# Kernel optimization log

Hardware: AMD Instinct MI355X
Metric: run time of the kernel (lower is better)

## Reference

```python
import jax, jax.numpy as jnp
import numpy as np

LAMBDA_1 = 0.1
LAMBDA_2 = 0.1
MAX_ITER = 200
EPS = 1e-5
L = 128   # out_size + 1
D = 512   # in_feature
M = 2048  # in_size


def make_delta(l):
    # second-difference matrix: lower-tri toeplitz of [1,-2,1], with [0,0]=0, [1,0]=-1
    Dm = (jnp.eye(l, dtype=jnp.float32)
          - 2.0 * jnp.eye(l, k=-1, dtype=jnp.float32)
          + jnp.eye(l, k=-2, dtype=jnp.float32))
    return Dm.at[0, 0].set(0.0).at[1, 0].set(-1.0)


def soft_threshold(z, t):
    return jnp.sign(z) * jnp.maximum(jnp.abs(z) - t, 0.0)


def hankel_to_scalar(Mx):
    # average anti-diagonals of an (l, m) matrix -> vector of length l+m-1
    l, m = Mx.shape
    n = l + m - 1
    idx = (jnp.arange(l)[:, None] + jnp.arange(m)[None, :]).reshape(-1)
    sums = jax.ops.segment_sum(Mx.reshape(-1), idx, num_segments=n)
    k = jnp.arange(n)
    counts = jnp.minimum(jnp.minimum(k + 1, n - k), min(l, m)).astype(Mx.dtype)
    return sums / counts


def nrmse(a, b):
    # normalized (relative) L2 error ||a-b|| / ||a||
    return jnp.linalg.norm(a - b) / jnp.linalg.norm(a)


def setup_inputs() -> dict:
    key = jax.random.key(0)
    k1, k2, k3, k4 = jax.random.split(key, 4)
    x = jax.random.normal(k1, (D, M), dtype=jnp.float32)
    part_y = jax.random.normal(k2, (L, M), dtype=jnp.float32)
    mask = (jax.random.uniform(k3, (L, M)) < 0.8).astype(jnp.float32)
    y0 = jax.random.uniform(k4, (L + M - 1,), dtype=jnp.float32)
    return {"x": x, "part_y": part_y, "mask": mask, "y0": y0}


def reference(x, part_y, mask, y0):
    d, m = x.shape
    l = part_y.shape[0]
    Delta = make_delta(l)
    DtD = Delta.T @ Delta
    max_sx = jnp.linalg.svd(x, compute_uv=False)[0] ** 2          # maxeig(x)
    eig = jnp.linalg.svd(Delta, compute_uv=False)[0] ** 2          # maxeig(Delta)
    tau = 1.0 / (2.0 * (max_sx + LAMBDA_1 * eig))
    lam2 = jnp.where(tau * LAMBDA_2 > 0.1, 0.1 / tau, LAMBDA_2)
    thr = tau * lam2
    tail = l - 1

    def update(A, B, a):
        G = LAMBDA_1 * (DtD @ A) + (mask * (A @ x - part_y)) @ x.T
        A_new = soft_threshold(B - tau * G, thr)
        a_new = (1.0 + jnp.sqrt(1.0 + 4.0 * a * a)) / 2.0
        B_new = A + (a - 1.0) / a_new * (A_new - A)
        return A_new, B_new, a_new

    def cond(state):
        _, _, _, _, it, done = state
        return jnp.logical_and(it < MAX_ITER, jnp.logical_not(done))

    def body(state):
        A, B, a, y_k, it, done = state
        A_new, B_new, a_new = update(A, B, a)
        ax = hankel_to_scalar(A_new @ x)
        conv = nrmse(y_k[-tail:], ax[-tail:])
        return (A_new, B_new, a_new, ax, it + 1, conv <= EPS)

    A0 = jnp.zeros((l, d), dtype=x.dtype)
    state0 = (A0, A0, jnp.float32(1.0), y0, jnp.int32(0), jnp.array(False))
    A, _, _, _, _, _ = jax.lax.while_loop(cond, body, state0)
    return (A @ x, A)
```

## Files before the change

kernel.cpp:

```cpp
#include <hip/hip_runtime.h>
#include <math.h>


#define L 128
#define D 512
#define M 2048
#define TAIL (L - 1)
#define MAXIT 200
#define EPSV 1e-5f
#define LAM1 0.1f
#define LAM2C 0.1f
#define LD (L * D)

#define OFF_A     0
#define OFF_BM    131072
#define OFF_R     262144
#define OFF_AX    524288
#define OFF_P     786432
#define OFF_PAR   OFF_P
#define OFF_Q     1048576
#define OFF_DTD   1310720
#define OFF_DP    1327104
#define OFF_DQ    1343488
#define OFF_CTAB  1359872
#define OFF_YPREV 1360128
#define OFF_PART  1360256
#define OFF_WV    1362304
#define OFF_VV    1362816
#define OFF_T64   1363328
#define OFF_Y64   1367424
#define OFF_SCAL  1368448
#define OFF_WD    1368512
#define OFF_WD2   1368640

#define SC_MX    0
#define SC_MXD   24
#define SC_EIGD  44
#define SC_TAU   45
#define SC_THR   46
#define SI_DONE  48
#define SI_PAR   49

__device__ __forceinline__ float delta_elem(int i, int j) {
  if (i == 0) return 0.f;
  if (i == 1) return (j == 0) ? -1.f : (j == 1 ? 1.f : 0.f);
  return (j == i) ? 1.f : (j == i - 1 ? -2.f : (j == i - 2 ? 1.f : 0.f));
}

__global__ __launch_bounds__(256) void k_init(float* __restrict__ ws,
                                              const float* __restrict__ part_y,
                                              const float* __restrict__ mask,
                                              const float* __restrict__ y0) {
  int gid = blockIdx.x * blockDim.x + threadIdx.x;
  int stride = gridDim.x * blockDim.x;
  for (int i = gid; i < 4 * LD; i += stride) ws[OFF_A + i] = 0.f;
  for (int i = gid; i < L * M; i += stride) ws[OFF_R + i] = -mask[i] * part_y[i];
  for (int i = gid; i < L * L; i += stride) {
    int r = i / L, c = i % L;
    float s = 0.f;
    for (int k = 0; k < L; ++k) s += delta_elem(k, r) * delta_elem(k, c);
    ws[OFF_DTD + i] = s;
  }
  if (gid < TAIL) ws[OFF_YPREV + gid] = y0[M + gid];
  if (gid == 0) {
    for (int i = 0; i < 64; ++i) ws[OFF_SCAL + i] = 0.f;
    ws[OFF_SCAL + SC_MXD] = 6.0f;
    float a = 1.f;
    for (int t = 0; t < MAXIT; ++t) {
      float an = (1.f + sqrtf(1.f + 4.f * a * a)) * 0.5f;
      ws[OFF_CTAB + t] = (a - 1.f) / an;
      a = an;
    }
  }
}

__global__ __launch_bounds__(256) void k_xxt(const float* __restrict__ x,
                                             float* __restrict__ ws) {
  int bt = blockIdx.x;
  int r0 = (bt / 16) * 32, c0 = (bt % 16) * 32;
  int rr = threadIdx.x / 32, cl = threadIdx.x % 32;
  int c = c0 + cl;
  const float4* xc = (const float4*)(x + (size_t)c * M);
  float acc[4] = {0.f, 0.f, 0.f, 0.f};
  for (int m4 = 0; m4 < M / 4; ++m4) {
    float4 b = xc[m4];
#pragma unroll
    for (int k = 0; k < 4; ++k) {
      float4 a = ((const float4*)(x + (size_t)(r0 + rr + 8 * k) * M))[m4];
      acc[k] += a.x * b.x + a.y * b.y + a.z * b.z + a.w * b.w;
    }
  }
  float* P = ws + OFF_P;
  float mloc = 0.f;
#pragma unroll
  for (int k = 0; k < 4; ++k) {
    P[(size_t)(r0 + rr + 8 * k) * D + c] = acc[k];
    mloc = fmaxf(mloc, fabsf(acc[k]));
  }
  __shared__ float sm[256];
  sm[threadIdx.x] = mloc; __syncthreads();
  for (int s = 128; s > 0; s >>= 1) {
    if ((int)threadIdx.x < s) sm[threadIdx.x] = fmaxf(sm[threadIdx.x], sm[threadIdx.x + s]);
    __syncthreads();
  }
  if (threadIdx.x == 0) atomicMax((int*)(ws + OFF_SCAL + SC_MX), __float_as_int(sm[0]));
}

template <int N, int TILES>
__global__ __launch_bounds__(256) void k_sq(const float* __restrict__ src,
                                            float* __restrict__ dst,
                                            float* __restrict__ ws,
                                            int slotIn, int slotOut) {
  float sc = 1.0f / ws[OFF_SCAL + slotIn];
  int bt = blockIdx.x;
  int r0 = (bt / TILES) * 32, c0 = (bt % TILES) * 32;
  int rr = threadIdx.x / 32, cl = threadIdx.x % 32;
  int c = c0 + cl;
  const float4* bc = (const float4*)(src + (size_t)c * N);
  float acc[4] = {0.f, 0.f, 0.f, 0.f};
  for (int m4 = 0; m4 < N / 4; ++m4) {
    float4 b = bc[m4];
#pragma unroll
    for (int k = 0; k < 4; ++k) {
      float4 a = ((const float4*)(src + (size_t)(r0 + rr + 8 * k) * N))[m4];
      acc[k] += a.x * b.x + a.y * b.y + a.z * b.z + a.w * b.w;
    }
  }
  float mloc = 0.f;
#pragma unroll
  for (int k = 0; k < 4; ++k) {
    float v = acc[k] * sc * sc;
    dst[(size_t)(r0 + rr + 8 * k) * N + c] = v;
    mloc = fmaxf(mloc, fabsf(v));
  }
  __shared__ float sm[256];
  sm[threadIdx.x] = mloc; __syncthreads();
  for (int s = 128; s > 0; s >>= 1) {
    if ((int)threadIdx.x < s) sm[threadIdx.x] = fmaxf(sm[threadIdx.x], sm[threadIdx.x + s]);
    __syncthreads();
  }
  if (threadIdx.x == 0) atomicMax((int*)(ws + OFF_SCAL + slotOut), __float_as_int(sm[0]));
}

template <int N>
__global__ __launch_bounds__(64) void k_mv(const float* __restrict__ P,
                                           const float* __restrict__ vin,
                                           float* __restrict__ vout, int useVec) {
  int i = blockIdx.x * 64 + threadIdx.x;
  const float4* Pr = (const float4*)(P + (size_t)i * N);
  float acc = 0.f;
  if (useVec) {
    const float4* v4 = (const float4*)vin;
    for (int j = 0; j < N / 4; ++j) {
      float4 a = Pr[j]; float4 b = v4[j];
      acc += a.x * b.x + a.y * b.y + a.z * b.z + a.w * b.w;
    }
  } else {
    for (int j = 0; j < N / 4; ++j) { float4 a = Pr[j]; acc += a.x + a.y + a.z + a.w; }
  }
  vout[i] = acc;
}

__global__ __launch_bounds__(128) void k_xtv(const float* __restrict__ x,
                                             const float* __restrict__ v,
                                             double* __restrict__ t) {
  int m = blockIdx.x * blockDim.x + threadIdx.x;
  double acc = 0.0;
  for (int i = 0; i < D; ++i) acc += (double)x[(size_t)i * M + m] * (double)v[i];
  t[m] = acc;
}

__global__ __launch_bounds__(64) void k_xt(const float* __restrict__ x,
                                           const double* __restrict__ t,
                                           double* __restrict__ y) {
  int i = blockIdx.x * blockDim.x + threadIdx.x;
  double acc = 0.0;
  for (int m = 0; m < M; ++m) acc += (double)x[(size_t)i * M + m] * t[m];
  y[i] = acc;
}

__global__ __launch_bounds__(512) void k_tau(float* __restrict__ ws) {
  const double* y = (const double*)(ws + OFF_Y64);
  const float* v = ws + OFF_VV;
  __shared__ double sn[512], sd[512];
  int i = threadIdx.x;
  double vi = (double)v[i];
  sn[i] = vi * y[i];
  sd[i] = vi * vi;
  __syncthreads();
  for (int s = 256; s > 0; s >>= 1) {
    if (i < s) { sn[i] += sn[i + s]; sd[i] += sd[i + s]; }
    __syncthreads();
  }
  if (i == 0) {
    float max_sx = (float)(sn[0] / sd[0]);
    float eigD = ws[OFF_SCAL + SC_EIGD];
    float tau = 1.0f / (2.0f * (max_sx + LAM1 * eigD));
    float lam2 = (tau * LAM2C > 0.1f) ? 0.1f / tau : LAM2C;
    ws[OFF_SCAL + SC_TAU] = tau;
    ws[OFF_SCAL + SC_THR] = tau * lam2;
  }
}

__global__ __launch_bounds__(128) void k_eigd(float* __restrict__ ws) {
  int i = threadIdx.x;
  const float* DtD = ws + OFF_DTD;
  const float* v = ws + OFF_WD2;
  float acc = 0.f;
  for (int j = 0; j < L; ++j) acc += DtD[i * L + j] * v[j];
  __shared__ float sn[128], sd[128];
  sn[i] = acc * v[i]; sd[i] = v[i] * v[i];
  __syncthreads();
  for (int s = 64; s > 0; s >>= 1) {
    if (i < s) { sn[i] += sn[i + s]; sd[i] += sd[i + s]; }
    __syncthreads();
  }
  if (i == 0) ws[OFF_SCAL + SC_EIGD] = sn[0] / sd[0];
}

__global__ __launch_bounds__(256) void k1p(const float* __restrict__ x,
                                           float* __restrict__ ws, int t) {
  int* iscal = (int*)(ws + OFF_SCAL);
  if (iscal[SI_DONE]) return;
  int chunk = blockIdx.x >> 6;
  int tile = blockIdx.x & 63;
  int rt = tile >> 3, ct = tile & 7;
  int tid = threadIdx.x;
  int w = tid >> 6, lane = tid & 63;
  int r0 = rt * 16 + w * 4;
  int c = ct * 64 + lane;

  if (chunk == 7 && tile == 0 && t >= 1) {
    __shared__ float snum[128], sden[128];
    if (tid < TAIL) {
      float s = 0.f;
#pragma unroll
      for (int slot = 0; slot < 16; ++slot) s += ws[OFF_PART + slot * 128 + tid];
      float ax = s / (float)(TAIL - tid);
      float yp = ws[OFF_YPREV + tid];
      float d = yp - ax;
      snum[tid] = d * d;
      sden[tid] = yp * yp;
      ws[OFF_YPREV + tid] = ax;
    }
    __syncthreads();
    if (tid == 0) {
      float num = 0.f, den = 0.f;
      for (int k = 0; k < TAIL; ++k) { num += snum[k]; den += sden[k]; }
      float conv = sqrtf(num) / sqrtf(den);
      if (conv <= EPSV) { iscal[SI_DONE] = 1; iscal[SI_PAR] = t & 1; }
    }
  }

  float acc0 = 0.f, acc1 = 0.f, acc2 = 0.f, acc3 = 0.f;
  {
    const float4* xr = (const float4*)(x + (size_t)c * M) + chunk * 64;
    const float4* R0 = (const float4*)(ws + OFF_R + (size_t)(r0 + 0) * M) + chunk * 64;
    const float4* R1 = (const float4*)(ws + OFF_R + (size_t)(r0 + 1) * M) + chunk * 64;
    const float4* R2 = (const float4*)(ws + OFF_R + (size_t)(r0 + 2) * M) + chunk * 64;
    const float4* R3 = (const float4*)(ws + OFF_R + (size_t)(r0 + 3) * M) + chunk * 64;
#pragma unroll 4
    for (int i = 0; i < 64; ++i) {
      float4 b = xr[i];
      float4 a0 = R0[i], a1 = R1[i], a2 = R2[i], a3 = R3[i];
      acc0 += a0.x * b.x + a0.y * b.y + a0.z * b.z + a0.w * b.w;
      acc1 += a1.x * b.x + a1.y * b.y + a1.z * b.z + a1.w * b.w;
      acc2 += a2.x * b.x + a2.y * b.y + a2.z * b.z + a2.w * b.w;
      acc3 += a3.x * b.x + a3.y * b.y + a3.z * b.z + a3.w * b.w;
    }
  }
  if (chunk == 7) {
    const float4* D0 = (const float4*)(ws + OFF_DTD + (size_t)(r0 + 0) * L);
    const float4* D1 = (const float4*)(ws + OFF_DTD + (size_t)(r0 + 1) * L);
    const float4* D2 = (const float4*)(ws + OFF_DTD + (size_t)(r0 + 2) * L);
    const float4* D3 = (const float4*)(ws + OFF_DTD + (size_t)(r0 + 3) * L);
    const float* Ab = ws + OFF_A + (size_t)(t & 1) * LD;
    float g0 = 0.f, g1 = 0.f, g2 = 0.f, g3 = 0.f;
#pragma unroll 2
    for (int p4 = 0; p4 < 32; ++p4) {
      float4 d0 = D0[p4], d1 = D1[p4], d2 = D2[p4], d3 = D3[p4];
      float ap0 = Ab[(size_t)(p4 * 4 + 0) * D + c];
      float ap1 = Ab[(size_t)(p4 * 4 + 1) * D + c];
      float ap2 = Ab[(size_t)(p4 * 4 + 2) * D + c];
      float ap3 = Ab[(size_t)(p4 * 4 + 3) * D + c];
      g0 += d0.x * ap0 + d0.y * ap1 + d0.z * ap2 + d0.w * ap3;
      g1 += d1.x * ap0 + d1.y * ap1 + d1.z * ap2 + d1.w * ap3;
      g2 += d2.x * ap0 + d2.y * ap1 + d2.z * ap2 + d2.w * ap3;
      g3 += d3.x * ap0 + d3.y * ap1 + d3.z * ap2 + d3.w * ap3;
    }
    acc0 += LAM1 * g0; acc1 += LAM1 * g1; acc2 += LAM1 * g2; acc3 += LAM1 * g3;
  }
  float* P = ws + OFF_PAR + (size_t)chunk * LD;
  P[(size_t)(r0 + 0) * D + c] = acc0;
  P[(size_t)(r0 + 1) * D + c] = acc1;
  P[(size_t)(r0 + 2) * D + c] = acc2;
  P[(size_t)(r0 + 3) * D + c] = acc3;
}

__global__ __launch_bounds__(256) void k1b(float* __restrict__ ws, int t) {
  int* iscal = (int*)(ws + OFF_SCAL);
  if (iscal[SI_DONE]) return;
  int idx = blockIdx.x * 256 + threadIdx.x;
  float g = 0.f;
#pragma unroll
  for (int ch = 0; ch < 8; ++ch) g += ws[OFF_PAR + ch * LD + idx];
  float tau = ws[OFF_SCAL + SC_TAU];
  float thr = ws[OFF_SCAL + SC_THR];
  float ctv = ws[OFF_CTAB + t];
  float aold = ws[OFF_A + (t & 1) * LD + idx];
  float bm = ws[OFF_BM + (t & 1) * LD + idx];
  float z = bm - tau * g;
  float az = fabsf(z) - thr;
  float anew = az > 0.f ? copysignf(az, z) : 0.f;
  ws[OFF_A + ((t + 1) & 1) * LD + idx] = anew;
  ws[OFF_BM + ((t + 1) & 1) * LD + idx] = aold + ctv * (anew - aold);
}

__global__ __launch_bounds__(512) void k2(const float* __restrict__ x,
                                          const float* __restrict__ py,
                                          const float* __restrict__ mask,
                                          float* __restrict__ ws, int t) {
  int* iscal = (int*)(ws + OFF_SCAL);
  if (iscal[SI_DONE]) return;
  int bid = blockIdx.x;
  int rt = bid >> 5, ct = bid & 31;
  int tid = threadIdx.x;
  int half = tid >> 8;
  int w2 = (tid >> 6) & 3;
  int lane = tid & 63;
  int r0 = rt * 16 + w2 * 4;
  int c = ct * 64 + lane;
  const float* A = ws + OFF_A + (size_t)((t + 1) & 1) * LD;
  float acc0 = 0.f, acc1 = 0.f, acc2 = 0.f, acc3 = 0.f;
  int d4lo = half * 64;
#pragma unroll 2
  for (int d4 = d4lo; d4 < d4lo + 64; ++d4) {
    float xs0 = x[(size_t)(d4 * 4 + 0) * M + c];
    float xs1 = x[(size_t)(d4 * 4 + 1) * M + c];
    float xs2 = x[(size_t)(d4 * 4 + 2) * M + c];
    float xs3 = x[(size_t)(d4 * 4 + 3) * M + c];
    float4 a0 = ((const float4*)(A + (size_t)(r0 + 0) * D))[d4];
    float4 a1 = ((const float4*)(A + (size_t)(r0 + 1) * D))[d4];
    float4 a2 = ((const float4*)(A + (size_t)(r0 + 2) * D))[d4];
    float4 a3 = ((const float4*)(A + (size_t)(r0 + 3) * D))[d4];
    acc0 += a0.x * xs0 + a0.y * xs1 + a0.z * xs2 + a0.w * xs3;
    acc1 += a1.x * xs0 + a1.y * xs1 + a1.z * xs2 + a1.w * xs3;
    acc2 += a2.x * xs0 + a2.y * xs1 + a2.z * xs2 + a2.w * xs3;
    acc3 += a3.x * xs0 + a3.y * xs1 + a3.z * xs2 + a3.w * xs3;
  }
  __shared__ float tile[16][65];
  if (half == 0) {
    tile[w2 * 4 + 0][lane] = acc0;
    tile[w2 * 4 + 1][lane] = acc1;
    tile[w2 * 4 + 2][lane] = acc2;
    tile[w2 * 4 + 3][lane] = acc3;
  }
  __syncthreads();
  if (half == 1) {
    float s0 = tile[w2 * 4 + 0][lane] + acc0;
    float s1 = tile[w2 * 4 + 1][lane] + acc1;
    float s2 = tile[w2 * 4 + 2][lane] + acc2;
    float s3 = tile[w2 * 4 + 3][lane] + acc3;
    size_t o0 = (size_t)(r0 + 0) * M + c;
    size_t o1 = (size_t)(r0 + 1) * M + c;
    size_t o2 = (size_t)(r0 + 2) * M + c;
    size_t o3 = (size_t)(r0 + 3) * M + c;
    ws[OFF_AX + o0] = s0; ws[OFF_R + o0] = mask[o0] * (s0 - py[o0]);
    ws[OFF_AX + o1] = s1; ws[OFF_R + o1] = mask[o1] * (s1 - py[o1]);
    ws[OFF_AX + o2] = s2; ws[OFF_R + o2] = mask[o2] * (s2 - py[o2]);
    ws[OFF_AX + o3] = s3; ws[OFF_R + o3] = mask[o3] * (s3 - py[o3]);
    tile[w2 * 4 + 0][lane] = s0;
    tile[w2 * 4 + 1][lane] = s1;
    tile[w2 * 4 + 2][lane] = s2;
    tile[w2 * 4 + 3][lane] = s3;
  }
  if (ct >= 30) {
    __syncthreads();
    int slot = rt * 2 + (ct - 30);
    if (tid < TAIL) {
      int kk = M + tid;
      int rbase = rt * 16, c0 = ct * 64;
      int rlo = max(rbase, kk - (c0 + 63));
      int rhi = min(rbase + 15, kk - c0);
      float s = 0.f;
      for (int r = rlo; r <= rhi; ++r) s += tile[r - rbase][(kk - r) - c0];
      ws[OFF_PART + slot * 128 + tid] = s;
    }
  }
}

__global__ __launch_bounds__(256) void k_final(const float* __restrict__ ws,
                                               float* __restrict__ out) {
  const int* iscal = (const int*)(ws + OFF_SCAL);
  int par = iscal[SI_PAR];
  int gid = blockIdx.x * blockDim.x + threadIdx.x;
  int stride = gridDim.x * blockDim.x;
  for (int i = gid; i < L * M; i += stride) out[i] = ws[OFF_AX + i];
  for (int i = gid; i < LD; i += stride) out[L * M + i] = ws[OFF_A + par * LD + i];
}

extern "C" void kernel_launch(void* const* d_in, const int* in_sizes, int n_in,
                              void* d_out, int out_size, void* d_ws, size_t ws_size,
                              hipStream_t stream) {
  (void)in_sizes; (void)n_in; (void)out_size; (void)ws_size;
  const float* x = (const float*)d_in[0];
  const float* py = (const float*)d_in[1];
  const float* mk = (const float*)d_in[2];
  const float* y0 = (const float*)d_in[3];
  float* out = (float*)d_out;
  float* ws = (float*)d_ws;

  float* gP = ws + OFF_P;
  float* gQ = ws + OFF_Q;
  float* dP = ws + OFF_DP;
  float* dQ = ws + OFF_DQ;
  float* gDtD = ws + OFF_DTD;

  k_init<<<256, 256, 0, stream>>>(ws, py, mk, y0);

  k_xxt<<<256, 256, 0, stream>>>(x, ws);
  for (int s = 0; s < 12; ++s) {
    const float* src = (s % 2 == 0) ? gP : gQ;
    float* dst = (s % 2 == 0) ? gQ : gP;
    k_sq<512, 16><<<256, 256, 0, stream>>>(src, dst, ws, SC_MX + s, SC_MX + s + 1);
  }
  k_mv<512><<<8, 64, 0, stream>>>(gP, nullptr, ws + OFF_WV, 0);
  k_mv<512><<<8, 64, 0, stream>>>(gP, ws + OFF_WV, ws + OFF_VV, 1);
  k_mv<512><<<8, 64, 0, stream>>>(gP, ws + OFF_VV, ws + OFF_WV, 1);
  k_mv<512><<<8, 64, 0, stream>>>(gP, ws + OFF_WV, ws + OFF_VV, 1);
  k_xtv<<<16, 128, 0, stream>>>(x, ws + OFF_VV, (double*)(ws + OFF_T64));
  k_xt<<<8, 64, 0, stream>>>(x, (const double*)(ws + OFF_T64), (double*)(ws + OFF_Y64));

  for (int s = 0; s < 10; ++s) {
    const float* src = (s == 0) ? gDtD : ((s % 2 == 1) ? dP : dQ);
    float* dst = (s % 2 == 0) ? dP : dQ;
    k_sq<128, 4><<<16, 256, 0, stream>>>(src, dst, ws, SC_MXD + s, SC_MXD + s + 1);
  }
  k_mv<128><<<2, 64, 0, stream>>>(dQ, nullptr, ws + OFF_WD, 0);
  k_mv<128><<<2, 64, 0, stream>>>(dQ, ws + OFF_WD, ws + OFF_WD2, 2);
  k_eigd<<<1, 128, 0, stream>>>(ws);
  k_tau<<<1, 512, 0, stream>>>(ws);

  for (int t = 0; t < MAXIT; ++t) {
    k1p<<<512, 256, 0, stream>>>(x, ws, t);
    k1b<<<256, 256, 0, stream>>>(ws, t);
    k2<<<256, 512, 0, stream>>>(x, py, mk, ws, t);
  }

  k_final<<<256, 256, 0, stream>>>(ws, out);
}
```

Baseline: 12.38 ms.

## Fuse setup and iteration loop into persistent kernels with grid barriers

Replaces the long sequence of small launches (setup squarings, power iterations, and three kernels per FISTA iteration) with two persistent kernels, k_setup and k_loop. These use a software grid barrier built on atomics over 256 blocks of 512 threads. The gradient is recomputed per output tile with split-K inside the block instead of partial buffers plus a reduction kernel. The goal is to remove launch overhead and the partial-sum round trips. The risk is that the spin barrier deadlocks if not all 256 blocks are co-resident, and the barriers themselves add latency.

```diff
diff --git a/kernel.cpp b/kernel.cpp
--- a/kernel.cpp
+++ b/kernel.cpp
@@ -11,13 +11,14 @@
 #define LAM1 0.1f
 #define LAM2C 0.1f
 #define LD (L * D)
+#define NBLK 256
+#define NTHR 512
 
 #define OFF_A     0
 #define OFF_BM    131072
 #define OFF_R     262144
 #define OFF_AX    524288
 #define OFF_P     786432
-#define OFF_PAR   OFF_P
 #define OFF_Q     1048576
 #define OFF_DTD   1310720
 #define OFF_DP    1327104
@@ -30,8 +31,6 @@
 #define OFF_T64   1363328
 #define OFF_Y64   1367424
 #define OFF_SCAL  1368448
-#define OFF_WD    1368512
-#define OFF_WD2   1368640
 
 #define SC_MX    0
 #define SC_MXD   24
@@ -39,12 +38,33 @@
 #define SC_TAU   45
 #define SC_THR   46
 #define SI_DONE  48
-#define SI_PAR   49
+#define SI_CNT   52
+#define SI_GEN   53
 
 __device__ __forceinline__ float delta_elem(int i, int j) {
   if (i == 0) return 0.f;
   if (i == 1) return (j == 0) ? -1.f : (j == 1 ? 1.f : 0.f);
   return (j == i) ? 1.f : (j == i - 1 ? -2.f : (j == i - 2 ? 1.f : 0.f));
+}
+
+__device__ __forceinline__ void gbar(float* ws) {
+  __syncthreads();
+  if (threadIdx.x == 0) {
+    unsigned* cnt = (unsigned*)(ws + OFF_SCAL) + SI_CNT;
+    unsigned* gen = (unsigned*)(ws + OFF_SCAL) + SI_GEN;
+    __threadfence();
+    unsigned g = __hip_atomic_load(gen, __ATOMIC_RELAXED, __HIP_MEMORY_SCOPE_AGENT);
+    unsigned a = __hip_atomic_fetch_add(cnt, 1u, __ATOMIC_ACQ_REL, __HIP_MEMORY_SCOPE_AGENT);
+    if (a == NBLK - 1) {
+      __hip_atomic_store(cnt, 0u, __ATOMIC_RELAXED, __HIP_MEMORY_SCOPE_AGENT);
+      __hip_atomic_store(gen, g + 1u, __ATOMIC_RELEASE, __HIP_MEMORY_SCOPE_AGENT);
+    } else {
+      while (__hip_atomic_load(gen, __ATOMIC_ACQUIRE, __HIP_MEMORY_SCOPE_AGENT) == g)
+        __builtin_amdgcn_s_sleep(2);
+    }
+    __threadfence();
+  }
+  __syncthreads();
 }
 
 __global__ __launch_bounds__(256) void k_init(float* __restrict__ ws,
@@ -74,329 +94,347 @@
   }
 }
 
-__global__ __launch_bounds__(256) void k_xxt(const float* __restrict__ x,
-                                             float* __restrict__ ws) {
-  int bt = blockIdx.x;
-  int r0 = (bt / 16) * 32, c0 = (bt % 16) * 32;
-  int rr = threadIdx.x / 32, cl = threadIdx.x % 32;
-  int c = c0 + cl;
-  const float4* xc = (const float4*)(x + (size_t)c * M);
-  float acc[4] = {0.f, 0.f, 0.f, 0.f};
-  for (int m4 = 0; m4 < M / 4; ++m4) {
-    float4 b = xc[m4];
-#pragma unroll
-    for (int k = 0; k < 4; ++k) {
-      float4 a = ((const float4*)(x + (size_t)(r0 + rr + 8 * k) * M))[m4];
-      acc[k] += a.x * b.x + a.y * b.y + a.z * b.z + a.w * b.w;
-    }
-  }
-  float* P = ws + OFF_P;
-  float mloc = 0.f;
-#pragma unroll
-  for (int k = 0; k < 4; ++k) {
-    P[(size_t)(r0 + rr + 8 * k) * D + c] = acc[k];
-    mloc = fmaxf(mloc, fabsf(acc[k]));
-  }
-  __shared__ float sm[256];
-  sm[threadIdx.x] = mloc; __syncthreads();
-  for (int s = 128; s > 0; s >>= 1) {
-    if ((int)threadIdx.x < s) sm[threadIdx.x] = fmaxf(sm[threadIdx.x], sm[threadIdx.x + s]);
-    __syncthreads();
-  }
-  if (threadIdx.x == 0) atomicMax((int*)(ws + OFF_SCAL + SC_MX), __float_as_int(sm[0]));
-}
-
 template <int N, int TILES>
-__global__ __launch_bounds__(256) void k_sq(const float* __restrict__ src,
-                                            float* __restrict__ dst,
-                                            float* __restrict__ ws,
-                                            int slotIn, int slotOut) {
-  float sc = 1.0f / ws[OFF_SCAL + slotIn];
-  int bt = blockIdx.x;
+__device__ __forceinline__ void sq_step(const float* __restrict__ src,
+                                        float* __restrict__ dst,
+                                        float* __restrict__ scal,
+                                        int si, int so, float* sm, int bt) {
+  float sc = 1.0f / scal[si];
   int r0 = (bt / TILES) * 32, c0 = (bt % TILES) * 32;
-  int rr = threadIdx.x / 32, cl = threadIdx.x % 32;
+  int rr = threadIdx.x >> 5, cl = threadIdx.x & 31;
   int c = c0 + cl;
   const float4* bc = (const float4*)(src + (size_t)c * N);
-  float acc[4] = {0.f, 0.f, 0.f, 0.f};
+  const float4* a0p = (const float4*)(src + (size_t)(r0 + rr) * N);
+  const float4* a1p = (const float4*)(src + (size_t)(r0 + rr + 16) * N);
+  float a0 = 0.f, a1 = 0.f;
   for (int m4 = 0; m4 < N / 4; ++m4) {
     float4 b = bc[m4];
-#pragma unroll
-    for (int k = 0; k < 4; ++k) {
-      float4 a = ((const float4*)(src + (size_t)(r0 + rr + 8 * k) * N))[m4];
-      acc[k] += a.x * b.x + a.y * b.y + a.z * b.z + a.w * b.w;
-    }
-  }
-  float mloc = 0.f;
-#pragma unroll
-  for (int k = 0; k < 4; ++k) {
-    float v = acc[k] * sc * sc;
-    dst[(size_t)(r0 + rr + 8 * k) * N + c] = v;
-    mloc = fmaxf(mloc, fabsf(v));
-  }
-  __shared__ float sm[256];
-  sm[threadIdx.x] = mloc; __syncthreads();
-  for (int s = 128; s > 0; s >>= 1) {
-    if ((int)threadIdx.x < s) sm[threadIdx.x] = fmaxf(sm[threadIdx.x], sm[threadIdx.x + s]);
-    __syncthreads();
-  }
-  if (threadIdx.x == 0) atomicMax((int*)(ws + OFF_SCAL + slotOut), __float_as_int(sm[0]));
-}
-
-template <int N>
-__global__ __launch_bounds__(64) void k_mv(const float* __restrict__ P,
-                                           const float* __restrict__ vin,
-                                           float* __restrict__ vout, int useVec) {
-  int i = blockIdx.x * 64 + threadIdx.x;
-  const float4* Pr = (const float4*)(P + (size_t)i * N);
-  float acc = 0.f;
-  if (useVec) {
-    const float4* v4 = (const float4*)vin;
-    for (int j = 0; j < N / 4; ++j) {
-      float4 a = Pr[j]; float4 b = v4[j];
-      acc += a.x * b.x + a.y * b.y + a.z * b.z + a.w * b.w;
-    }
-  } else {
-    for (int j = 0; j < N / 4; ++j) { float4 a = Pr[j]; acc += a.x + a.y + a.z + a.w; }
-  }
-  vout[i] = acc;
-}
-
-__global__ __launch_bounds__(128) void k_xtv(const float* __restrict__ x,
-                                             const float* __restrict__ v,
-                                             double* __restrict__ t) {
-  int m = blockIdx.x * blockDim.x + threadIdx.x;
-  double acc = 0.0;
-  for (int i = 0; i < D; ++i) acc += (double)x[(size_t)i * M + m] * (double)v[i];
-  t[m] = acc;
-}
-
-__global__ __launch_bounds__(64) void k_xt(const float* __restrict__ x,
-                                           const double* __restrict__ t,
-                                           double* __restrict__ y) {
-  int i = blockIdx.x * blockDim.x + threadIdx.x;
-  double acc = 0.0;
-  for (int m = 0; m < M; ++m) acc += (double)x[(size_t)i * M + m] * t[m];
-  y[i] = acc;
-}
-
-__global__ __launch_bounds__(512) void k_tau(float* __restrict__ ws) {
-  const double* y = (const double*)(ws + OFF_Y64);
-  const float* v = ws + OFF_VV;
-  __shared__ double sn[512], sd[512];
-  int i = threadIdx.x;
-  double vi = (double)v[i];
-  sn[i] = vi * y[i];
-  sd[i] = vi * vi;
+    float4 p = a0p[m4], q = a1p[m4];
+    a0 += p.x * b.x + p.y * b.y + p.z * b.z + p.w * b.w;
+    a1 += q.x * b.x + q.y * b.y + q.z * b.z + q.w * b.w;
+  }
+  a0 *= sc * sc; a1 *= sc * sc;
+  dst[(size_t)(r0 + rr) * N + c] = a0;
+  dst[(size_t)(r0 + rr + 16) * N + c] = a1;
+  sm[threadIdx.x] = fmaxf(fabsf(a0), fabsf(a1));
   __syncthreads();
   for (int s = 256; s > 0; s >>= 1) {
-    if (i < s) { sn[i] += sn[i + s]; sd[i] += sd[i + s]; }
-    __syncthreads();
-  }
-  if (i == 0) {
-    float max_sx = (float)(sn[0] / sd[0]);
-    float eigD = ws[OFF_SCAL + SC_EIGD];
-    float tau = 1.0f / (2.0f * (max_sx + LAM1 * eigD));
-    float lam2 = (tau * LAM2C > 0.1f) ? 0.1f / tau : LAM2C;
-    ws[OFF_SCAL + SC_TAU] = tau;
-    ws[OFF_SCAL + SC_THR] = tau * lam2;
-  }
-}
-
-__global__ __launch_bounds__(128) void k_eigd(float* __restrict__ ws) {
-  int i = threadIdx.x;
-  const float* DtD = ws + OFF_DTD;
-  const float* v = ws + OFF_WD2;
-  float acc = 0.f;
-  for (int j = 0; j < L; ++j) acc += DtD[i * L + j] * v[j];
-  __shared__ float sn[128], sd[128];
-  sn[i] = acc * v[i]; sd[i] = v[i] * v[i];
-  __syncthreads();
-  for (int s = 64; s > 0; s >>= 1) {
-    if (i < s) { sn[i] += sn[i + s]; sd[i] += sd[i + s]; }
-    __syncthreads();
-  }
-  if (i == 0) ws[OFF_SCAL + SC_EIGD] = sn[0] / sd[0];
-}
-
-__global__ __launch_bounds__(256) void k1p(const float* __restrict__ x,
-                                           float* __restrict__ ws, int t) {
+    if ((int)threadIdx.x < s) sm[threadIdx.x] = fmaxf(sm[threadIdx.x], sm[threadIdx.x + s]);
+    __syncthreads();
+  }
+  if (threadIdx.x == 0) atomicMax((int*)(scal + so), __float_as_int(sm[0]));
+}
+
+__global__ __launch_bounds__(NTHR, 2) void k_setup(const float* __restrict__ x,
+                                                   float* __restrict__ ws) {
+  const int tid = threadIdx.x, bid = blockIdx.x;
+  __shared__ float sm[NTHR];
+  __shared__ double sdn[NTHR], sdd[NTHR];
+  float* scal = ws + OFF_SCAL;
+
+  {
+    int r0 = (bid >> 4) * 32, c0 = (bid & 15) * 32;
+    int rr = tid >> 5, cl = tid & 31;
+    int c = c0 + cl;
+    const float4* xc = (const float4*)(x + (size_t)c * M);
+    const float4* xr0 = (const float4*)(x + (size_t)(r0 + rr) * M);
+    const float4* xr1 = (const float4*)(x + (size_t)(r0 + rr + 16) * M);
+    float a0 = 0.f, a1 = 0.f;
+    for (int m4 = 0; m4 < M / 4; ++m4) {
+      float4 b = xc[m4];
+      float4 p = xr0[m4], q = xr1[m4];
+      a0 += p.x * b.x + p.y * b.y + p.z * b.z + p.w * b.w;
+      a1 += q.x * b.x + q.y * b.y + q.z * b.z + q.w * b.w;
+    }
+    float* P = ws + OFF_P;
+    P[(size_t)(r0 + rr) * D + c] = a0;
+    P[(size_t)(r0 + rr + 16) * D + c] = a1;
+    sm[tid] = fmaxf(fabsf(a0), fabsf(a1));
+    __syncthreads();
+    for (int s = 256; s > 0; s >>= 1) {
+      if (tid < s) sm[tid] = fmaxf(sm[tid], sm[tid + s]);
+      __syncthreads();
+    }
+    if (tid == 0) atomicMax((int*)(scal + SC_MX), __float_as_int(sm[0]));
+  }
+  gbar(ws);
+
+  for (int s = 0; s < 12; ++s) {
+    if (bid < 16 && s < 10) {
+      const float* src = (s == 0) ? ws + OFF_DTD : ((s & 1) ? ws + OFF_DP : ws + OFF_DQ);
+      float* dst = (s & 1) ? ws + OFF_DQ : ws + OFF_DP;
+      sq_step<128, 4>(src, dst, scal, SC_MXD + s, SC_MXD + s + 1, sm, bid);
+    }
+    __syncthreads();
+    {
+      const float* src = (s & 1) ? ws + OFF_Q : ws + OFF_P;
+      float* dst = (s & 1) ? ws + OFF_P : ws + OFF_Q;
+      sq_step<512, 16>(src, dst, scal, SC_MX + s, SC_MX + s + 1, sm, bid);
+    }
+    gbar(ws);
+  }
+
+  const float* gP = ws + OFF_P;
+  const float* dQ = ws + OFF_DQ;
+  if (bid == 0) {
+    const float4* Pr = (const float4*)(gP + (size_t)tid * D);
+    float a = 0.f;
+    for (int j = 0; j < D / 4; ++j) { float4 v = Pr[j]; a += v.x + v.y + v.z + v.w; }
+    ws[OFF_WV + tid] = a;
+  }
+  if (bid == 1 && tid < L) {
+    const float4* Dr = (const float4*)(dQ + (size_t)tid * L);
+    float a = 0.f;
+    for (int j = 0; j < L / 4; ++j) { float4 v = Dr[j]; a += v.x + v.y + v.z + v.w; }
+    ws[OFF_WV + 512 + tid] = a;
+  }
+  gbar(ws);
+  if (bid == 0) {
+    const float4* Pr = (const float4*)(gP + (size_t)tid * D);
+    const float4* v4 = (const float4*)(ws + OFF_WV);
+    float a = 0.f;
+    for (int j = 0; j < D / 4; ++j) {
+      float4 p = Pr[j]; float4 v = v4[j];
+      a += p.x * v.x + p.y * v.y + p.z * v.z + p.w * v.w;
+    }
+    ws[OFF_VV + tid] = a;
+  }
+  if (bid == 1 && tid < L) {
+    const float* wd = ws + OFF_WV + 512;
+    const float* Dr = dQ + (size_t)tid * L;
+    float a = 0.f;
+    for (int j = 0; j < L; ++j) a += Dr[j] * wd[j];
+    ws[OFF_WV + 640 + tid] = a;
+  }
+  gbar(ws);
+  if (bid == 0) {
+    const float4* Pr = (const float4*)(gP + (size_t)tid * D);
+    const float4* v4 = (const float4*)(ws + OFF_VV);
+    float a = 0.f;
+    for (int j = 0; j < D / 4; ++j) {
+      float4 p = Pr[j]; float4 v = v4[j];
+      a += p.x * v.x + p.y * v.y + p.z * v.z + p.w * v.w;
+    }
+    ws[OFF_WV + tid] = a;
+  }
+  if (bid == 1) {
+    float accv = 0.f, vv = 0.f;
+    if (tid < L) {
+      const float* v = ws + OFF_WV + 640;
+      const float* DtD = ws + OFF_DTD;
+      for (int j = 0; j < L; ++j) accv += DtD[(size_t)tid * L + j] * v[j];
+      vv = v[tid];
+    }
+    sm[tid] = (tid < L) ? accv * vv : 0.f;
+    sm[256 + (tid & 255)] = 0.f;
+    __syncthreads();
+    if (tid < L) sm[256 + tid] = vv * vv;
+    __syncthreads();
+    if (tid == 0) {
+      float n = 0.f, d = 0.f;
+      for (int k = 0; k < L; ++k) { n += sm[k]; d += sm[256 + k]; }
+      scal[SC_EIGD] = n / d;
+    }
+  }
+  gbar(ws);
+  if (bid == 0) {
+    const float4* Pr = (const float4*)(gP + (size_t)tid * D);
+    const float4* v4 = (const float4*)(ws + OFF_WV);
+    float a = 0.f;
+    for (int j = 0; j < D / 4; ++j) {
+      float4 p = Pr[j]; float4 v = v4[j];
+      a += p.x * v.x + p.y * v.y + p.z * v.z + p.w * v.w;
+    }
+    ws[OFF_VV + tid] = a;
+  }
+  gbar(ws);
+  if (bid < 4) {
+    int m = bid * NTHR + tid;
+    double acc = 0.0;
+    for (int i = 0; i < D; ++i) acc += (double)x[(size_t)i * M + m] * (double)ws[OFF_VV + i];
+    ((double*)(ws + OFF_T64))[m] = acc;
+  }
+  gbar(ws);
+  if (bid == 0) {
+    const double* t64 = (const double*)(ws + OFF_T64);
+    double acc = 0.0;
+    for (int m = 0; m < M; ++m) acc += (double)x[(size_t)tid * M + m] * t64[m];
+    ((double*)(ws + OFF_Y64))[tid] = acc;
+  }
+  gbar(ws);
+  if (bid == 0) {
+    const double* y = (const double*)(ws + OFF_Y64);
+    double vi = (double)ws[OFF_VV + tid];
+    sdn[tid] = vi * y[tid];
+    sdd[tid] = vi * vi;
+    __syncthreads();
+    for (int s = 256; s > 0; s >>= 1) {
+      if (tid < s) { sdn[tid] += sdn[tid + s]; sdd[tid] += sdd[tid + s]; }
+      __syncthreads();
+    }
+    if (tid == 0) {
+      float max_sx = (float)(sdn[0] / sdd[0]);
+      float eigD = scal[SC_EIGD];
+      float tau = 1.0f / (2.0f * (max_sx + LAM1 * eigD));
+      float lam2 = (tau * LAM2C > 0.1f) ? 0.1f / tau : LAM2C;
+      scal[SC_TAU] = tau;
+      scal[SC_THR] = tau * lam2;
+    }
+  }
+}
+
+__global__ __launch_bounds__(NTHR, 2) void k_loop(const float* __restrict__ x,
+                                                  const float* __restrict__ py,
+                                                  const float* __restrict__ mask,
+                                                  float* __restrict__ ws,
+                                                  float* __restrict__ out) {
+  __shared__ float g2buf[256];
+  __shared__ float tile[16][65];
+  __shared__ float snum[128], sden[128];
+  __shared__ int flag;
+  const int tid = threadIdx.x, bid = blockIdx.x;
   int* iscal = (int*)(ws + OFF_SCAL);
-  if (iscal[SI_DONE]) return;
-  int chunk = blockIdx.x >> 6;
-  int tile = blockIdx.x & 63;
-  int rt = tile >> 3, ct = tile & 7;
-  int tid = threadIdx.x;
-  int w = tid >> 6, lane = tid & 63;
-  int r0 = rt * 16 + w * 4;
-  int c = ct * 64 + lane;
-
-  if (chunk == 7 && tile == 0 && t >= 1) {
-    __shared__ float snum[128], sden[128];
-    if (tid < TAIL) {
-      float s = 0.f;
+  const float tau = ws[OFF_SCAL + SC_TAU];
+  const float thr = ws[OFF_SCAL + SC_THR];
+  int par = 0;
+
+  for (int t = 0; t < MAXIT; ++t) {
+    if (bid == 0 && t >= 1) {
+      if (tid < TAIL) {
+        float s = 0.f;
 #pragma unroll
-      for (int slot = 0; slot < 16; ++slot) s += ws[OFF_PART + slot * 128 + tid];
-      float ax = s / (float)(TAIL - tid);
-      float yp = ws[OFF_YPREV + tid];
-      float d = yp - ax;
-      snum[tid] = d * d;
-      sden[tid] = yp * yp;
-      ws[OFF_YPREV + tid] = ax;
-    }
-    __syncthreads();
-    if (tid == 0) {
-      float num = 0.f, den = 0.f;
-      for (int k = 0; k < TAIL; ++k) { num += snum[k]; den += sden[k]; }
-      float conv = sqrtf(num) / sqrtf(den);
-      if (conv <= EPSV) { iscal[SI_DONE] = 1; iscal[SI_PAR] = t & 1; }
-    }
-  }
-
-  float acc0 = 0.f, acc1 = 0.f, acc2 = 0.f, acc3 = 0.f;
+        for (int slot = 0; slot < 16; ++slot) s += ws[OFF_PART + slot * 128 + tid];
+        float ax = s / (float)(TAIL - tid);
+        float yp = ws[OFF_YPREV + tid];
+        float d0 = yp - ax;
+        snum[tid] = d0 * d0;
+        sden[tid] = yp * yp;
+        ws[OFF_YPREV + tid] = ax;
+      }
+      __syncthreads();
+      if (tid == 0) {
+        float num = 0.f, den = 0.f;
+        for (int k = 0; k < TAIL; ++k) { num += snum[k]; den += sden[k]; }
+        float conv = sqrtf(num) / sqrtf(den);
+        if (conv <= EPSV) iscal[SI_DONE] = 1;
+      }
+      __syncthreads();
+    }
+    {
+      int rt = bid >> 4, ct = bid & 15;
+      int oi = tid & 255;
+      int r = rt * 8 + (oi >> 5);
+      int c = ct * 32 + (oi & 31);
+      int half = tid >> 8;
+      const float4* Rp = (const float4*)(ws + OFF_R + (size_t)r * M) + half * 256;
+      const float4* Xp = (const float4*)(x + (size_t)c * M) + half * 256;
+      float a0 = 0.f, a1 = 0.f;
+#pragma unroll 4
+      for (int i = 0; i < 256; i += 2) {
+        float4 ra = Rp[i], xa = Xp[i];
+        float4 rb = Rp[i + 1], xb = Xp[i + 1];
+        a0 += ra.x * xa.x + ra.y * xa.y + ra.z * xa.z + ra.w * xa.w;
+        a1 += rb.x * xb.x + rb.y * xb.y + rb.z * xb.z + rb.w * xb.w;
+      }
+      float g2 = a0 + a1;
+      if (half) g2buf[oi] = g2;
+      __syncthreads();
+      if (!half) {
+        const float* Ao = ws + OFF_A + (size_t)(t & 1) * LD;
+        const float4* Dr = (const float4*)(ws + OFF_DTD + (size_t)r * L);
+        float gd = 0.f;
+#pragma unroll 4
+        for (int p4 = 0; p4 < 32; ++p4) {
+          float4 dv = Dr[p4];
+          gd += dv.x * Ao[(size_t)(p4 * 4 + 0) * D + c] + dv.y * Ao[(size_t)(p4 * 4 + 1) * D + c] +
+                dv.z * Ao[(size_t)(p4 * 4 + 2) * D + c] + dv.w * Ao[(size_t)(p4 * 4 + 3) * D + c];
+        }
+        float g = g2 + g2buf[oi] + LAM1 * gd;
+        float ctv = ws[OFF_CTAB + t];
+        size_t off = (size_t)r * D + c;
+        float aold = Ao[off];
+        float bm = ws[OFF_BM + (size_t)(t & 1) * LD + off];
+        float z = bm - tau * g;
+        float az = fabsf(z) - thr;
+        float anew = az > 0.f ? copysignf(az, z) : 0.f;
+        ws[OFF_A + (size_t)((t + 1) & 1) * LD + off] = anew;
+        ws[OFF_BM + (size_t)((t + 1) & 1) * LD + off] = aold + ctv * (anew - aold);
+      }
+    }
+    gbar(ws);
+    if (tid == 0) flag = __hip_atomic_load(iscal + SI_DONE, __ATOMIC_RELAXED, __HIP_MEMORY_SCOPE_AGENT);
+    __syncthreads();
+    if (flag) { par = t & 1; break; }
+    {
+      int rt = bid >> 5, ct = bid & 31;
+      int half = tid >> 8, w2 = (tid >> 6) & 3, lane = tid & 63;
+      int r0 = rt * 16 + w2 * 4;
+      int c = ct * 64 + lane;
+      const float* A = ws + OFF_A + (size_t)((t + 1) & 1) * LD;
+      float acc0 = 0.f, acc1 = 0.f, acc2 = 0.f, acc3 = 0.f;
+      int d4lo = half * 64;
+#pragma unroll 2
+      for (int d4 = d4lo; d4 < d4lo + 64; ++d4) {
+        float xs0 = x[(size_t)(d4 * 4 + 0) * M + c];
+        float xs1 = x[(size_t)(d4 * 4 + 1) * M + c];
+        float xs2 = x[(size_t)(d4 * 4 + 2) * M + c];
+        float xs3 = x[(size_t)(d4 * 4 + 3) * M + c];
+        float4 a0v = ((const float4*)(A + (size_t)(r0 + 0) * D))[d4];
+        float4 a1v = ((const float4*)(A + (size_t)(r0 + 1) * D))[d4];
+        float4 a2v = ((const float4*)(A + (size_t)(r0 + 2) * D))[d4];
+        float4 a3v = ((const float4*)(A + (size_t)(r0 + 3) * D))[d4];
+        acc0 += a0v.x * xs0 + a0v.y * xs1 + a0v.z * xs2 + a0v.w * xs3;
+        acc1 += a1v.x * xs0 + a1v.y * xs1 + a1v.z * xs2 + a1v.w * xs3;
+        acc2 += a2v.x * xs0 + a2v.y * xs1 + a2v.z * xs2 + a2v.w * xs3;
+        acc3 += a3v.x * xs0 + a3v.y * xs1 + a3v.z * xs2 + a3v.w * xs3;
+      }
+      if (half == 0) {
+        tile[w2 * 4 + 0][lane] = acc0;
+        tile[w2 * 4 + 1][lane] = acc1;
+        tile[w2 * 4 + 2][lane] = acc2;
+        tile[w2 * 4 + 3][lane] = acc3;
+      }
+      __syncthreads();
+      if (half == 1) {
+        float s0 = tile[w2 * 4 + 0][lane] + acc0;
+        float s1 = tile[w2 * 4 + 1][lane] + acc1;
+        float s2 = tile[w2 * 4 + 2][lane] + acc2;
+        float s3 = tile[w2 * 4 + 3][lane] + acc3;
+        size_t o0 = (size_t)(r0 + 0) * M + c;
+        size_t o1 = (size_t)(r0 + 1) * M + c;
+        size_t o2 = (size_t)(r0 + 2) * M + c;
+        size_t o3 = (size_t)(r0 + 3) * M + c;
+        ws[OFF_AX + o0] = s0; ws[OFF_R + o0] = mask[o0] * (s0 - py[o0]);
+        ws[OFF_AX + o1] = s1; ws[OFF_R + o1] = mask[o1] * (s1 - py[o1]);
+        ws[OFF_AX + o2] = s2; ws[OFF_R + o2] = mask[o2] * (s2 - py[o2]);
+        ws[OFF_AX + o3] = s3; ws[OFF_R + o3] = mask[o3] * (s3 - py[o3]);
+        tile[w2 * 4 + 0][lane] = s0;
+        tile[w2 * 4 + 1][lane] = s1;
+        tile[w2 * 4 + 2][lane] = s2;
+        tile[w2 * 4 + 3][lane] = s3;
+      }
+      if (ct >= 30) {
+        __syncthreads();
+        int slot = rt * 2 + (ct - 30);
+        if (tid < TAIL) {
+          int kk = M + tid;
+          int rbase = rt * 16, c0 = ct * 64;
+          int rlo = max(rbase, kk - (c0 + 63));
+          int rhi = min(rbase + 15, kk - c0);
+          float s = 0.f;
+          for (int r = rlo; r <= rhi; ++r) s += tile[r - rbase][(kk - r) - c0];
+          ws[OFF_PART + slot * 128 + tid] = s;
+        }
+      }
+    }
+    gbar(ws);
+  }
+
   {
-    const float4* xr = (const float4*)(x + (size_t)c * M) + chunk * 64;
-    const float4* R0 = (const float4*)(ws + OFF_R + (size_t)(r0 + 0) * M) + chunk * 64;
-    const float4* R1 = (const float4*)(ws + OFF_R + (size_t)(r0 + 1) * M) + chunk * 64;
-    const float4* R2 = (const float4*)(ws + OFF_R + (size_t)(r0 + 2) * M) + chunk * 64;
-    const float4* R3 = (const float4*)(ws + OFF_R + (size_t)(r0 + 3) * M) + chunk * 64;
-#pragma unroll 4
-    for (int i = 0; i < 64; ++i) {
-      float4 b = xr[i];
-      float4 a0 = R0[i], a1 = R1[i], a2 = R2[i], a3 = R3[i];
-      acc0 += a0.x * b.x + a0.y * b.y + a0.z * b.z + a0.w * b.w;
-      acc1 += a1.x * b.x + a1.y * b.y + a1.z * b.z + a1.w * b.w;
-      acc2 += a2.x * b.x + a2.y * b.y + a2.z * b.z + a2.w * b.w;
-      acc3 += a3.x * b.x + a3.y * b.y + a3.z * b.z + a3.w * b.w;
-    }
-  }
-  if (chunk == 7) {
-    const float4* D0 = (const float4*)(ws + OFF_DTD + (size_t)(r0 + 0) * L);
-    const float4* D1 = (const float4*)(ws + OFF_DTD + (size_t)(r0 + 1) * L);
-    const float4* D2 = (const float4*)(ws + OFF_DTD + (size_t)(r0 + 2) * L);
-    const float4* D3 = (const float4*)(ws + OFF_DTD + (size_t)(r0 + 3) * L);
-    const float* Ab = ws + OFF_A + (size_t)(t & 1) * LD;
-    float g0 = 0.f, g1 = 0.f, g2 = 0.f, g3 = 0.f;
-#pragma unroll 2
-    for (int p4 = 0; p4 < 32; ++p4) {
-      float4 d0 = D0[p4], d1 = D1[p4], d2 = D2[p4], d3 = D3[p4];
-      float ap0 = Ab[(size_t)(p4 * 4 + 0) * D + c];
-      float ap1 = Ab[(size_t)(p4 * 4 + 1) * D + c];
-      float ap2 = Ab[(size_t)(p4 * 4 + 2) * D + c];
-      float ap3 = Ab[(size_t)(p4 * 4 + 3) * D + c];
-      g0 += d0.x * ap0 + d0.y * ap1 + d0.z * ap2 + d0.w * ap3;
-      g1 += d1.x * ap0 + d1.y * ap1 + d1.z * ap2 + d1.w * ap3;
-      g2 += d2.x * ap0 + d2.y * ap1 + d2.z * ap2 + d2.w * ap3;
-      g3 += d3.x * ap0 + d3.y * ap1 + d3.z * ap2 + d3.w * ap3;
-    }
-    acc0 += LAM1 * g0; acc1 += LAM1 * g1; acc2 += LAM1 * g2; acc3 += LAM1 * g3;
-  }
-  float* P = ws + OFF_PAR + (size_t)chunk * LD;
-  P[(size_t)(r0 + 0) * D + c] = acc0;
-  P[(size_t)(r0 + 1) * D + c] = acc1;
-  P[(size_t)(r0 + 2) * D + c] = acc2;
-  P[(size_t)(r0 + 3) * D + c] = acc3;
-}
-
-__global__ __launch_bounds__(256) void k1b(float* __restrict__ ws, int t) {
-  int* iscal = (int*)(ws + OFF_SCAL);
-  if (iscal[SI_DONE]) return;
-  int idx = blockIdx.x * 256 + threadIdx.x;
-  float g = 0.f;
-#pragma unroll
-  for (int ch = 0; ch < 8; ++ch) g += ws[OFF_PAR + ch * LD + idx];
-  float tau = ws[OFF_SCAL + SC_TAU];
-  float thr = ws[OFF_SCAL + SC_THR];
-  float ctv = ws[OFF_CTAB + t];
-  float aold = ws[OFF_A + (t & 1) * LD + idx];
-  float bm = ws[OFF_BM + (t & 1) * LD + idx];
-  float z = bm - tau * g;
-  float az = fabsf(z) - thr;
-  float anew = az > 0.f ? copysignf(az, z) : 0.f;
-  ws[OFF_A + ((t + 1) & 1) * LD + idx] = anew;
-  ws[OFF_BM + ((t + 1) & 1) * LD + idx] = aold + ctv * (anew - aold);
-}
-
-__global__ __launch_bounds__(512) void k2(const float* __restrict__ x,
-                                          const float* __restrict__ py,
-                                          const float* __restrict__ mask,
-                                          float* __restrict__ ws, int t) {
-  int* iscal = (int*)(ws + OFF_SCAL);
-  if (iscal[SI_DONE]) return;
-  int bid = blockIdx.x;
-  int rt = bid >> 5, ct = bid & 31;
-  int tid = threadIdx.x;
-  int half = tid >> 8;
-  int w2 = (tid >> 6) & 3;
-  int lane = tid & 63;
-  int r0 = rt * 16 + w2 * 4;
-  int c = ct * 64 + lane;
-  const float* A = ws + OFF_A + (size_t)((t + 1) & 1) * LD;
-  float acc0 = 0.f, acc1 = 0.f, acc2 = 0.f, acc3 = 0.f;
-  int d4lo = half * 64;
-#pragma unroll 2
-  for (int d4 = d4lo; d4 < d4lo + 64; ++d4) {
-    float xs0 = x[(size_t)(d4 * 4 + 0) * M + c];
-    float xs1 = x[(size_t)(d4 * 4 + 1) * M + c];
-    float xs2 = x[(size_t)(d4 * 4 + 2) * M + c];
-    float xs3 = x[(size_t)(d4 * 4 + 3) * M + c];
-    float4 a0 = ((const float4*)(A + (size_t)(r0 + 0) * D))[d4];
-    float4 a1 = ((const float4*)(A + (size_t)(r0 + 1) * D))[d4];
-    float4 a2 = ((const float4*)(A + (size_t)(r0 + 2) * D))[d4];
-    float4 a3 = ((const float4*)(A + (size_t)(r0 + 3) * D))[d4];
-    acc0 += a0.x * xs0 + a0.y * xs1 + a0.z * xs2 + a0.w * xs3;
-    acc1 += a1.x * xs0 + a1.y * xs1 + a1.z * xs2 + a1.w * xs3;
-    acc2 += a2.x * xs0 + a2.y * xs1 + a2.z * xs2 + a2.w * xs3;
-    acc3 += a3.x * xs0 + a3.y * xs1 + a3.z * xs2 + a3.w * xs3;
-  }
-  __shared__ float tile[16][65];
-  if (half == 0) {
-    tile[w2 * 4 + 0][lane] = acc0;
-    tile[w2 * 4 + 1][lane] = acc1;
-    tile[w2 * 4 + 2][lane] = acc2;
-    tile[w2 * 4 + 3][lane] = acc3;
-  }
-  __syncthreads();
-  if (half == 1) {
-    float s0 = tile[w2 * 4 + 0][lane] + acc0;
-    float s1 = tile[w2 * 4 + 1][lane] + acc1;
-    float s2 = tile[w2 * 4 + 2][lane] + acc2;
-    float s3 = tile[w2 * 4 + 3][lane] + acc3;
-    size_t o0 = (size_t)(r0 + 0) * M + c;
-    size_t o1 = (size_t)(r0 + 1) * M + c;
-    size_t o2 = (size_t)(r0 + 2) * M + c;
-    size_t o3 = (size_t)(r0 + 3) * M + c;
-    ws[OFF_AX + o0] = s0; ws[OFF_R + o0] = mask[o0] * (s0 - py[o0]);
-    ws[OFF_AX + o1] = s1; ws[OFF_R + o1] = mask[o1] * (s1 - py[o1]);
-    ws[OFF_AX + o2] = s2; ws[OFF_R + o2] = mask[o2] * (s2 - py[o2]);
-    ws[OFF_AX + o3] = s3; ws[OFF_R + o3] = mask[o3] * (s3 - py[o3]);
-    tile[w2 * 4 + 0][lane] = s0;
-    tile[w2 * 4 + 1][lane] = s1;
-    tile[w2 * 4 + 2][lane] = s2;
-    tile[w2 * 4 + 3][lane] = s3;
-  }
-  if (ct >= 30) {
-    __syncthreads();
-    int slot = rt * 2 + (ct - 30);
-    if (tid < TAIL) {
-      int kk = M + tid;
-      int rbase = rt * 16, c0 = ct * 64;
-      int rlo = max(rbase, kk - (c0 + 63));
-      int rhi = min(rbase + 15, kk - c0);
-      float s = 0.f;
-      for (int r = rlo; r <= rhi; ++r) s += tile[r - rbase][(kk - r) - c0];
-      ws[OFF_PART + slot * 128 + tid] = s;
-    }
-  }
-}
-
-__global__ __launch_bounds__(256) void k_final(const float* __restrict__ ws,
-                                               float* __restrict__ out) {
-  const int* iscal = (const int*)(ws + OFF_SCAL);
-  int par = iscal[SI_PAR];
-  int gid = blockIdx.x * blockDim.x + threadIdx.x;
-  int stride = gridDim.x * blockDim.x;
-  for (int i = gid; i < L * M; i += stride) out[i] = ws[OFF_AX + i];
-  for (int i = gid; i < LD; i += stride) out[L * M + i] = ws[OFF_A + par * LD + i];
+    int gid = bid * NTHR + tid;
+    for (int i = gid; i < L * M; i += NBLK * NTHR) out[i] = ws[OFF_AX + i];
+    for (int i = gid; i < LD; i += NBLK * NTHR) out[L * M + i] = ws[OFF_A + (size_t)par * LD + i];
+  }
 }
 
 extern "C" void kernel_launch(void* const* d_in, const int* in_sizes, int n_in,
@@ -410,42 +448,7 @@
   float* out = (float*)d_out;
   float* ws = (float*)d_ws;
 
-  float* gP = ws + OFF_P;
-  float* gQ = ws + OFF_Q;
-  float* dP = ws + OFF_DP;
-  float* dQ = ws + OFF_DQ;
-  float* gDtD = ws + OFF_DTD;
-
   k_init<<<256, 256, 0, stream>>>(ws, py, mk, y0);
-
-  k_xxt<<<256, 256, 0, stream>>>(x, ws);
-  for (int s = 0; s < 12; ++s) {
-    const float* src = (s % 2 == 0) ? gP : gQ;
-    float* dst = (s % 2 == 0) ? gQ : gP;
-    k_sq<512, 16><<<256, 256, 0, stream>>>(src, dst, ws, SC_MX + s, SC_MX + s + 1);
-  }
-  k_mv<512><<<8, 64, 0, stream>>>(gP, nullptr, ws + OFF_WV, 0);
-  k_mv<512><<<8, 64, 0, stream>>>(gP, ws + OFF_WV, ws + OFF_VV, 1);
-  k_mv<512><<<8, 64, 0, stream>>>(gP, ws + OFF_VV, ws + OFF_WV, 1);
-  k_mv<512><<<8, 64, 0, stream>>>(gP, ws + OFF_WV, ws + OFF_VV, 1);
-  k_xtv<<<16, 128, 0, stream>>>(x, ws + OFF_VV, (double*)(ws + OFF_T64));
-  k_xt<<<8, 64, 0, stream>>>(x, (const double*)(ws + OFF_T64), (double*)(ws + OFF_Y64));
-
-  for (int s = 0; s < 10; ++s) {
-    const float* src = (s == 0) ? gDtD : ((s % 2 == 1) ? dP : dQ);
-    float* dst = (s % 2 == 0) ? dP : dQ;
-    k_sq<128, 4><<<16, 256, 0, stream>>>(src, dst, ws, SC_MXD + s, SC_MXD + s + 1);
-  }
-  k_mv<128><<<2, 64, 0, stream>>>(dQ, nullptr, ws + OFF_WD, 0);
-  k_mv<128><<<2, 64, 0, stream>>>(dQ, ws + OFF_WD, ws + OFF_WD2, 2);
-  k_eigd<<<1, 128, 0, stream>>>(ws);
-  k_tau<<<1, 512, 0, stream>>>(ws);
-
-  for (int t = 0; t < MAXIT; ++t) {
-    k1p<<<512, 256, 0, stream>>>(x, ws, t);
-    k1b<<<256, 256, 0, stream>>>(ws, t);
-    k2<<<256, 512, 0, stream>>>(x, py, mk, ws, t);
-  }
-
-  k_final<<<256, 256, 0, stream>>>(ws, out);
-}
+  k_setup<<<NBLK, NTHR, 0, stream>>>(x, ws);
+  k_loop<<<NBLK, NTHR, 0, stream>>>(x, py, mk, ws, out);
+}
```

After: 37.51 ms. +203.1%, slower.
